# Kernel optimization log

Measured on AMD Instinct MI355X. Metric: run time of the kernel, lower is better.

The kernel has to match this reference:

```python
import jax, jax.numpy as jnp
import numpy as np

B, N, M, C = 1024, 2048, 128, 512
EPS = 1e-8


def setup_inputs() -> dict:
    key = jax.random.key(0)
    k1, k2, k3, k4, k5 = jax.random.split(key, 5)
    x = jax.random.normal(k1, (B, C), dtype=jnp.float32)
    u = jax.random.uniform(k2, (B, N), dtype=jnp.float32) + 1e-3
    w_prev = u / jnp.sum(u, axis=1, keepdims=True)  # valid attention distribution
    mem = jax.random.normal(k3, (B, N, M), dtype=jnp.float32)
    # xavier-uniform-ish fc_read weight (gain 1.4), tiny-std bias
    limit = 1.4 * np.sqrt(6.0 / (C + (M + 6)))
    W = jax.random.uniform(k4, (M + 6, C), dtype=jnp.float32, minval=-limit, maxval=limit)
    b = 0.01 * jax.random.normal(k5, (M + 6,), dtype=jnp.float32)
    return {"x": x, "w_prev": w_prev, "mem": mem, "W": W, "b": b}


def reference(x, w_prev, mem, W, b):
    m = mem.shape[-1]
    o = x @ W.T + b                                   # [B, M+6]
    k = o[:, :m]                                      # key [B, M]
    beta = jax.nn.softplus(o[:, m:m + 1])             # [B, 1]
    g = jax.nn.sigmoid(o[:, m + 1:m + 2])             # [B, 1]
    s = jax.nn.softmax(o[:, m + 2:m + 5], axis=1)     # [B, 3] shift weights
    gamma = 1.0 + jax.nn.softplus(o[:, m + 5:m + 6])  # [B, 1]

    # content addressing: cosine similarity, beta-sharpened softmax
    dot = jnp.einsum('bnm,bm->bn', mem, k)
    denom = jnp.linalg.norm(mem, axis=-1) * jnp.linalg.norm(k, axis=-1, keepdims=True) + EPS
    w_c = jax.nn.softmax(beta * (dot / denom), axis=1)  # [B, N]

    # gate interpolation
    w_g = g * w_c + (1.0 - g) * w_prev

    # circular convolution with 3-tap shift: w_t[i] = sum_j s[j] * w_g[(i+j-1) mod N]
    w_t = (s[:, 0:1] * jnp.roll(w_g, 1, axis=1)
           + s[:, 1:2] * w_g
           + s[:, 2:3] * jnp.roll(w_g, -1, axis=1))

    # sharpening
    w_pow = w_t ** gamma
    w = w_pow / (jnp.sum(w_pow, axis=1, keepdims=True) + 1e-16)

    # weighted read
    r = jnp.einsum('bn,bnm->bm', w, mem)
    return (r, w)
```

## Files before the change

kernel.cpp:

```cpp
#include <hip/hip_runtime.h>
#include <math.h>

#define B 1024
#define N 2048
#define M 128
#define C 512
#define OD (M + 6)
#define EPSF 1e-8f
#define CHUNK 512
#define NCHUNK 4
#define NGRP 64
#define ITERS (B / NGRP)
#define GRID_F (NCHUNK * NGRP)
#define AGENT __HIP_MEMORY_SCOPE_AGENT

__device__ __forceinline__ float softplusf(float x) {
    return fmaxf(x, 0.f) + log1pf(expf(-fabsf(x)));
}
__device__ __forceinline__ float sigmoidf_(float x) {
    return 1.f / (1.f + expf(-x));
}

__device__ __forceinline__ void bar_lds() {
    asm volatile("s_waitcnt lgkmcnt(0)" ::: "memory");
    __builtin_amdgcn_s_barrier();
}

__global__ __launch_bounds__(256) void k_head(
    const float* __restrict__ x, const float* __restrict__ W,
    const float* __restrict__ bias, float* __restrict__ kbuf,
    float* __restrict__ params)
{
    const int b = blockIdx.x;
    __shared__ float xs[C];
    __shared__ float os[OD];
    __shared__ float red[128];

    for (int i = threadIdx.x; i < C; i += 256) xs[i] = x[(size_t)b * C + i];
    __syncthreads();

    if (threadIdx.x < OD) {
        const int j = threadIdx.x;
        const float4* wr = (const float4*)(W + (size_t)j * C);
        float acc = 0.f;
#pragma unroll 8
        for (int c = 0; c < C / 4; ++c) {
            float4 wv = wr[c];
            acc = fmaf(wv.x, xs[4 * c + 0], acc);
            acc = fmaf(wv.y, xs[4 * c + 1], acc);
            acc = fmaf(wv.z, xs[4 * c + 2], acc);
            acc = fmaf(wv.w, xs[4 * c + 3], acc);
        }
        os[j] = acc + bias[j];
    }
    __syncthreads();

    if (threadIdx.x < M) {
        float v = os[threadIdx.x];
        kbuf[(size_t)b * M + threadIdx.x] = v;
        red[threadIdx.x] = v * v;
    }
    __syncthreads();
    for (int s = 64; s > 0; s >>= 1) {
        if (threadIdx.x < s) red[threadIdx.x] += red[threadIdx.x + s];
        __syncthreads();
    }
    if (threadIdx.x == 0) {
        float kn = sqrtf(red[0]);
        float beta = softplusf(os[M]);
        float g = sigmoidf_(os[M + 1]);
        float a0 = os[M + 2], a1 = os[M + 3], a2 = os[M + 4];
        float mx = fmaxf(a0, fmaxf(a1, a2));
        float e0 = expf(a0 - mx), e1 = expf(a1 - mx), e2 = expf(a2 - mx);
        float inv = 1.f / (e0 + e1 + e2);
        float gamma = 1.f + softplusf(os[M + 5]);
        float* p = params + (size_t)b * 8;
        p[0] = beta; p[1] = g; p[2] = e0 * inv; p[3] = e1 * inv;
        p[4] = e2 * inv; p[5] = gamma; p[6] = kn; p[7] = 0.f;
    }
}

__global__ __launch_bounds__(1024, 4) void k_fused(
    const float* __restrict__ mem, const float* __restrict__ kbuf,
    const float* __restrict__ params, const float* __restrict__ w_prev,
    float* __restrict__ w_out,
    float* __restrict__ sPart, float* __restrict__ tPart,
    int* __restrict__ cnt1, float* __restrict__ edgeE,
    float* __restrict__ rpart)
{
    __shared__ float eA[CHUNK];
    __shared__ float wgA[CHUNK + 2];
    __shared__ float pwA[CHUNK];
    __shared__ float redA[16 * 128];
    __shared__ float partS[32];
    __shared__ float partT[8];
    __shared__ float bcast[4];

    const int tid  = threadIdx.x;
    const int lane = tid & 63;
    const int wv   = tid >> 6;
    const int half = lane >> 5;
    const int l32  = lane & 31;
    const int hw   = wv * 2 + half;

    const int cid  = blockIdx.x >> 6;
    const int bgrp = blockIdx.x & 63;

    for (int it = 0; it < ITERS; ++it) {
        const int b = bgrp * ITERS + it;
        const float* cb = mem + ((size_t)b * N + cid * CHUNK) * M;

        float4 frag[16];
#pragma unroll
        for (int j = 0; j < 16; ++j)
            frag[j] = ((const float4*)(cb + (size_t)(hw * 16 + j) * M))[l32];

        float wp_t = 0.f, wpL = 0.f, wpR = 0.f;
        if (tid < CHUNK)
            wp_t = w_prev[(size_t)b * N + cid * CHUNK + tid];
        if (tid == 0) {
            wpL = w_prev[(size_t)b * N + ((cid * CHUNK + N - 1) & (N - 1))];
            wpR = w_prev[(size_t)b * N + ((cid * CHUNK + CHUNK) & (N - 1))];
        }
        const float4 kv = ((const float4*)(kbuf + (size_t)b * M))[l32];
        const float4 p0 = ((const float4*)(params + (size_t)b * 8))[0];
        const float4 p1 = ((const float4*)(params + (size_t)b * 8))[1];
        const float beta = p0.x, kn = p1.z;

        float myS = 0.f;
#pragma unroll
        for (int j = 0; j < 16; ++j) {
            float dot = frag[j].x * kv.x + frag[j].y * kv.y + frag[j].z * kv.z + frag[j].w * kv.w;
            float sq  = frag[j].x * frag[j].x + frag[j].y * frag[j].y + frag[j].z * frag[j].z + frag[j].w * frag[j].w;
#pragma unroll
            for (int s = 16; s >= 1; s >>= 1) {
                dot += __shfl_xor(dot, s, 64);
                sq  += __shfl_xor(sq,  s, 64);
            }
            if (l32 == 0) {
                const float z = beta * dot / (sqrtf(sq) * kn + EPSF);
                const float e = expf(z);
                eA[hw * 16 + j] = e;
                myS += e;
            }
        }
        if (l32 == 0) partS[hw] = myS;
        bar_lds();

        if (tid == 0) {
            float S = 0.f;
#pragma unroll
            for (int h = 0; h < 32; ++h) S += partS[h];
            __hip_atomic_store(&sPart[(size_t)b * NCHUNK + cid], S, __ATOMIC_RELAXED, AGENT);
            __hip_atomic_store(&edgeE[((size_t)b * NCHUNK + cid) * 2 + 0], eA[0], __ATOMIC_RELAXED, AGENT);
            __hip_atomic_store(&edgeE[((size_t)b * NCHUNK + cid) * 2 + 1], eA[CHUNK - 1], __ATOMIC_RELAXED, AGENT);
            asm volatile("s_waitcnt vmcnt(0)" ::: "memory");
            __hip_atomic_fetch_add(&cnt1[b], 1, __ATOMIC_RELAXED, AGENT);
            int tries = 0;
            while (__hip_atomic_load(&cnt1[b], __ATOMIC_RELAXED, AGENT) < NCHUNK) {
                __builtin_amdgcn_s_sleep(1);
                if (++tries > (1 << 22)) break;
            }
            float St = 0.f;
#pragma unroll
            for (int c2 = 0; c2 < NCHUNK; ++c2)
                St += __hip_atomic_load(&sPart[(size_t)b * NCHUNK + c2], __ATOMIC_RELAXED, AGENT);
            bcast[0] = 1.f / St;
            bcast[1] = __hip_atomic_load(&edgeE[((size_t)b * NCHUNK + ((cid + NCHUNK - 1) & (NCHUNK - 1))) * 2 + 1], __ATOMIC_RELAXED, AGENT);
            bcast[2] = __hip_atomic_load(&edgeE[((size_t)b * NCHUNK + ((cid + 1) & (NCHUNK - 1))) * 2 + 0], __ATOMIC_RELAXED, AGENT);
        }
        bar_lds();

        const float invS = bcast[0], eL = bcast[1], eR = bcast[2];
        const float g = p0.y, s0p = p0.z, s1p = p0.w, s2p = p1.x, gamma = p1.y;
        if (tid < CHUNK)
            wgA[tid + 1] = g * eA[tid] * invS + (1.f - g) * wp_t;
        if (tid == 0) {
            wgA[0]         = g * eL * invS + (1.f - g) * wpL;
            wgA[CHUNK + 1] = g * eR * invS + (1.f - g) * wpR;
        }
        bar_lds();

        float myT = 0.f;
        if (tid < CHUNK) {
            const float wt = s0p * wgA[tid] + s1p * wgA[tid + 1] + s2p * wgA[tid + 2];
            const float pw = powf(wt, gamma);
            pwA[tid] = pw;
            myT = pw;
        }
#pragma unroll
        for (int s = 32; s >= 1; s >>= 1) myT += __shfl_xor(myT, s, 64);
        if (lane == 0 && wv < 8) partT[wv] = myT;
        bar_lds();

        if (tid == 0) {
            float T = 0.f;
#pragma unroll
            for (int w2 = 0; w2 < 8; ++w2) T += partT[w2];
            tPart[(size_t)b * NCHUNK + cid] = T;
        }

        float4 acc = make_float4(0.f, 0.f, 0.f, 0.f);
#pragma unroll
        for (int j = 0; j < 16; ++j) {
            const float pw = pwA[hw * 16 + j];
            acc.x = fmaf(pw, frag[j].x, acc.x);
            acc.y = fmaf(pw, frag[j].y, acc.y);
            acc.z = fmaf(pw, frag[j].z, acc.z);
            acc.w = fmaf(pw, frag[j].w, acc.w);
        }
        acc.x += __shfl_xor(acc.x, 32, 64);
        acc.y += __shfl_xor(acc.y, 32, 64);
        acc.z += __shfl_xor(acc.z, 32, 64);
        acc.w += __shfl_xor(acc.w, 32, 64);
        if (half == 0) *(float4*)&redA[wv * 128 + l32 * 4] = acc;
        bar_lds();

        if (tid < 128) {
            float s = 0.f;
#pragma unroll
            for (int w2 = 0; w2 < 16; ++w2) s += redA[w2 * 128 + tid];
            rpart[((size_t)b * NCHUNK + cid) * 128 + tid] = s;
        }
        if (tid < CHUNK)
            w_out[(size_t)b * N + cid * CHUNK + tid] = pwA[tid];
        bar_lds();
    }
}

__global__ __launch_bounds__(256) void k_norm(
    const float* __restrict__ tPart, const float* __restrict__ rpart,
    float* __restrict__ w_out, float* __restrict__ r_out)
{
    const int b = blockIdx.x, tid = threadIdx.x;
    float T = 0.f;
#pragma unroll
    for (int c = 0; c < NCHUNK; ++c) T += tPart[(size_t)b * NCHUNK + c];
    const float invT = 1.f / (T + 1e-16f);

    float4* w4 = (float4*)(w_out + (size_t)b * N);
#pragma unroll
    for (int k = 0; k < 2; ++k) {
        float4 v = w4[tid + k * 256];
        v.x *= invT; v.y *= invT; v.z *= invT; v.w *= invT;
        w4[tid + k * 256] = v;
    }
    if (tid < 128) {
        float s = 0.f;
#pragma unroll
        for (int c = 0; c < NCHUNK; ++c)
            s += rpart[((size_t)b * NCHUNK + c) * 128 + tid];
        r_out[(size_t)b * M + tid] = s * invT;
    }
}

extern "C" void kernel_launch(void* const* d_in, const int* in_sizes, int n_in,
                              void* d_out, int out_size, void* d_ws, size_t ws_size,
                              hipStream_t stream) {
    const float* x      = (const float*)d_in[0];
    const float* w_prev = (const float*)d_in[1];
    const float* mem    = (const float*)d_in[2];
    const float* W      = (const float*)d_in[3];
    const float* bias   = (const float*)d_in[4];

    float* r_out = (float*)d_out;
    float* w_out = (float*)d_out + (size_t)B * M;

    float* ws     = (float*)d_ws;
    float* kbuf   = ws;
    float* params = kbuf + (size_t)B * M;
    float* sPart  = params + (size_t)B * 8;
    float* tPart  = sPart + (size_t)B * NCHUNK;
    int*   cnt1   = (int*)(tPart + (size_t)B * NCHUNK);
    float* edgeE  = (float*)(cnt1 + B);
    float* rpart  = edgeE + (size_t)B * NCHUNK * 2;

    hipMemsetAsync(cnt1, 0, B * sizeof(int), stream);

    k_head<<<B, 256, 0, stream>>>(x, W, bias, kbuf, params);
    k_fused<<<GRID_F, 1024, 0, stream>>>(mem, kbuf, params, w_prev, w_out,
                                         sPart, tPart, cnt1, edgeE, rpart);
    k_norm<<<B, 256, 0, stream>>>(tPart, rpart, w_out, r_out);
}
```

Before: 344.8 us.

## Double-buffer memory fragments across batch rows and halve block size

Each block now prefetches the next batch row's memory fragment, key and params into a second register set while the current row finishes, issuing the loads around the cross-block spin-wait so global latency overlaps the softmax-sum synchronisation. Chunking changes to 8 chunks of 256 rows with 512-thread blocks, keeping 256 blocks that each handle 32 rows. This doubles fragment register pressure (two float4[16] sets) and doubles the number of blocks that must meet at each per-row counter barrier.

```diff
diff --git a/kernel.cpp b/kernel.cpp
--- a/kernel.cpp
+++ b/kernel.cpp
@@ -7,11 +7,11 @@
 #define C 512
 #define OD (M + 6)
 #define EPSF 1e-8f
-#define CHUNK 512
-#define NCHUNK 4
-#define NGRP 64
-#define ITERS (B / NGRP)
-#define GRID_F (NCHUNK * NGRP)
+#define CHUNK 256
+#define NCHUNK 8
+#define NGRP 32
+#define ITERS 32
+#define GRID_F 256
 #define AGENT __HIP_MEMORY_SCOPE_AGENT
 
 __device__ __forceinline__ float softplusf(float x) {
@@ -80,7 +80,134 @@
     }
 }
 
-__global__ __launch_bounds__(1024, 4) void k_fused(
+#define STEP(IT, FC, KC, P0C, P1C, FN, KN_, P0N, P1N)                          \
+{                                                                              \
+    const int b  = bgrp * ITERS + (IT);                                        \
+    const int bn = (b + 1 < B) ? (b + 1) : b;   \
+    float wp_t = 0.f, wpL = 0.f, wpR = 0.f;                                    \
+    if (tid < CHUNK) wp_t = w_prev[(size_t)b * N + cid * CHUNK + tid];         \
+    if (tid == 0) {                                                            \
+        wpL = w_prev[(size_t)b * N + ((cid * CHUNK + N - 1) & (N - 1))];       \
+        wpR = w_prev[(size_t)b * N + ((cid * CHUNK + CHUNK) & (N - 1))];       \
+    }                                                                          \
+    const float beta = P0C.x, kn = P1C.z;                                      \
+                  \
+    float myS = 0.f;                                                           \
+    _Pragma("unroll")                                                          \
+    for (int j = 0; j < 16; ++j) {                                             \
+        float dot = FC[j].x * KC.x + FC[j].y * KC.y + FC[j].z * KC.z + FC[j].w * KC.w; \
+        float sq  = FC[j].x * FC[j].x + FC[j].y * FC[j].y + FC[j].z * FC[j].z + FC[j].w * FC[j].w; \
+        _Pragma("unroll")                                                      \
+        for (int s = 16; s >= 1; s >>= 1) {                                    \
+            dot += __shfl_xor(dot, s, 64);                                     \
+            sq  += __shfl_xor(sq,  s, 64);                                     \
+        }                                                                      \
+        if (l32 == 0) {                                                        \
+            const float z = beta * dot / (sqrtf(sq) * kn + EPSF);              \
+            const float e = expf(z);                                           \
+            eA[hw * 16 + j] = e;                                               \
+            myS += e;                                                          \
+        }                                                                      \
+    }                                                                          \
+    if (l32 == 0) partS[hw] = myS;                                             \
+    bar_lds();                                     \
+      \
+    if (tid == 0) {                                                            \
+        float S = 0.f;                                                         \
+        _Pragma("unroll")                                                      \
+        for (int h = 0; h < 16; ++h) S += partS[h];                            \
+        __hip_atomic_store(&sPart[(size_t)b * NCHUNK + cid], S, __ATOMIC_RELAXED, AGENT); \
+        __hip_atomic_store(&edgeE[((size_t)b * NCHUNK + cid) * 2 + 0], eA[0], __ATOMIC_RELAXED, AGENT); \
+        __hip_atomic_store(&edgeE[((size_t)b * NCHUNK + cid) * 2 + 1], eA[CHUNK - 1], __ATOMIC_RELAXED, AGENT); \
+        asm volatile("s_waitcnt vmcnt(0)" ::: "memory");                       \
+        __hip_atomic_fetch_add(&cnt1[b], 1, __ATOMIC_RELAXED, AGENT);          \
+    }                                                                          \
+     \
+    const float* nb = mem + ((size_t)bn * N + cid * CHUNK) * M;                \
+    if (wv != 0) {                                                             \
+        _Pragma("unroll")                                                      \
+        for (int j = 0; j < 16; ++j)                                           \
+            FN[j] = ((const float4*)(nb + (size_t)(hw * 16 + j) * M))[l32];    \
+        KN_ = ((const float4*)(kbuf + (size_t)bn * M))[l32];                   \
+    }                                                                          \
+    P0N = ((const float4*)(params + (size_t)bn * 8))[0];                       \
+    P1N = ((const float4*)(params + (size_t)bn * 8))[1];                       \
+         \
+    if (tid == 0) {                                                            \
+        int tries = 0;                                                         \
+        while (__hip_atomic_load(&cnt1[b], __ATOMIC_RELAXED, AGENT) < NCHUNK) {\
+            __builtin_amdgcn_s_sleep(1);                                       \
+            if (++tries > (1 << 22)) break;           \
+        }                                                                      \
+        float St = 0.f;                                                        \
+        _Pragma("unroll")                                                      \
+        for (int c2 = 0; c2 < NCHUNK; ++c2)    \
+            St += __hip_atomic_load(&sPart[(size_t)b * NCHUNK + c2], __ATOMIC_RELAXED, AGENT); \
+        bcast[0] = 1.f / St;                                                   \
+        bcast[1] = __hip_atomic_load(&edgeE[((size_t)b * NCHUNK + ((cid + NCHUNK - 1) & (NCHUNK - 1))) * 2 + 1], __ATOMIC_RELAXED, AGENT); \
+        bcast[2] = __hip_atomic_load(&edgeE[((size_t)b * NCHUNK + ((cid + 1) & (NCHUNK - 1))) * 2 + 0], __ATOMIC_RELAXED, AGENT); \
+    }                                                                          \
+    bar_lds();                                        \
+                               \
+    if (wv == 0) {                                                             \
+        _Pragma("unroll")                                                      \
+        for (int j = 0; j < 16; ++j)                                           \
+            FN[j] = ((const float4*)(nb + (size_t)(hw * 16 + j) * M))[l32];    \
+        KN_ = ((const float4*)(kbuf + (size_t)bn * M))[l32];                   \
+    }                                                                          \
+                             \
+    const float invS = bcast[0], eL = bcast[1], eR = bcast[2];                 \
+    const float g = P0C.y, s0p = P0C.z, s1p = P0C.w, s2p = P1C.x, gamma = P1C.y; \
+    if (tid < CHUNK)                                                           \
+        wgA[tid + 1] = g * eA[tid] * invS + (1.f - g) * wp_t;                  \
+    if (tid == 0) {                                                            \
+        wgA[0]         = g * eL * invS + (1.f - g) * wpL;                      \
+        wgA[CHUNK + 1] = g * eR * invS + (1.f - g) * wpR;                      \
+    }                                                                          \
+    bar_lds();                                          \
+    float myT = 0.f;                                                           \
+    if (tid < CHUNK) {                                                         \
+        const float wt = s0p * wgA[tid] + s1p * wgA[tid + 1] + s2p * wgA[tid + 2]; \
+        const float pw = powf(wt, gamma);                                      \
+        pwA[tid] = pw;                                                         \
+        myT = pw;                                                              \
+    }                                                                          \
+    _Pragma("unroll")                                                          \
+    for (int s = 32; s >= 1; s >>= 1) myT += __shfl_xor(myT, s, 64);           \
+    if (lane == 0 && wv < 4) partT[wv] = myT;                                  \
+    bar_lds();                                    \
+    if (tid == 0) {                                                            \
+        tPart[(size_t)b * NCHUNK + cid] = partT[0] + partT[1] + partT[2] + partT[3]; \
+    }                                                                          \
+       \
+    float4 acc = make_float4(0.f, 0.f, 0.f, 0.f);                              \
+    _Pragma("unroll")                                                          \
+    for (int j = 0; j < 16; ++j) {                                             \
+        const float pw = pwA[hw * 16 + j];                                     \
+        acc.x = fmaf(pw, FC[j].x, acc.x);                                      \
+        acc.y = fmaf(pw, FC[j].y, acc.y);                                      \
+        acc.z = fmaf(pw, FC[j].z, acc.z);                                      \
+        acc.w = fmaf(pw, FC[j].w, acc.w);                                      \
+    }                                                                          \
+    acc.x += __shfl_xor(acc.x, 32, 64);                                        \
+    acc.y += __shfl_xor(acc.y, 32, 64);                                        \
+    acc.z += __shfl_xor(acc.z, 32, 64);                                        \
+    acc.w += __shfl_xor(acc.w, 32, 64);                                        \
+    if (half == 0) *(float4*)&redA[wv * 128 + l32 * 4] = acc;                  \
+    bar_lds();                                         \
+    if (tid < 128) {                                                           \
+        float s = 0.f;                                                         \
+        _Pragma("unroll")                                                      \
+        for (int w2 = 0; w2 < 8; ++w2) s += redA[w2 * 128 + tid];              \
+        rpart[((size_t)b * NCHUNK + cid) * 128 + tid] = s;                     \
+    }                                                                          \
+                  \
+    if (tid < CHUNK)                                                           \
+        w_out[(size_t)b * N + cid * CHUNK + tid] = pwA[tid];                   \
+         \
+}
+
+__global__ __launch_bounds__(512, 2) void k_fused(
     const float* __restrict__ mem, const float* __restrict__ kbuf,
     const float* __restrict__ params, const float* __restrict__ w_prev,
     float* __restrict__ w_out,
@@ -91,9 +218,9 @@
     __shared__ float eA[CHUNK];
     __shared__ float wgA[CHUNK + 2];
     __shared__ float pwA[CHUNK];
-    __shared__ float redA[16 * 128];
-    __shared__ float partS[32];
-    __shared__ float partT[8];
+    __shared__ float redA[8 * 128];
+    __shared__ float partS[16];
+    __shared__ float partT[4];
     __shared__ float bcast[4];
 
     const int tid  = threadIdx.x;
@@ -103,128 +230,25 @@
     const int l32  = lane & 31;
     const int hw   = wv * 2 + half;
 
-    const int cid  = blockIdx.x >> 6;
-    const int bgrp = blockIdx.x & 63;
-
-    for (int it = 0; it < ITERS; ++it) {
-        const int b = bgrp * ITERS + it;
-        const float* cb = mem + ((size_t)b * N + cid * CHUNK) * M;
-
-        float4 frag[16];
+    const int cid  = blockIdx.x >> 5;
+    const int bgrp = blockIdx.x & 31;
+
+    float4 fA[16], fB[16], kvA, kvB, p0A, p1A, p0B, p1B;
+
+    {
+        const int b0 = bgrp * ITERS;
+        const float* cb = mem + ((size_t)b0 * N + cid * CHUNK) * M;
 #pragma unroll
         for (int j = 0; j < 16; ++j)
-            frag[j] = ((const float4*)(cb + (size_t)(hw * 16 + j) * M))[l32];
-
-        float wp_t = 0.f, wpL = 0.f, wpR = 0.f;
-        if (tid < CHUNK)
-            wp_t = w_prev[(size_t)b * N + cid * CHUNK + tid];
-        if (tid == 0) {
-            wpL = w_prev[(size_t)b * N + ((cid * CHUNK + N - 1) & (N - 1))];
-            wpR = w_prev[(size_t)b * N + ((cid * CHUNK + CHUNK) & (N - 1))];
-        }
-        const float4 kv = ((const float4*)(kbuf + (size_t)b * M))[l32];
-        const float4 p0 = ((const float4*)(params + (size_t)b * 8))[0];
-        const float4 p1 = ((const float4*)(params + (size_t)b * 8))[1];
-        const float beta = p0.x, kn = p1.z;
-
-        float myS = 0.f;
-#pragma unroll
-        for (int j = 0; j < 16; ++j) {
-            float dot = frag[j].x * kv.x + frag[j].y * kv.y + frag[j].z * kv.z + frag[j].w * kv.w;
-            float sq  = frag[j].x * frag[j].x + frag[j].y * frag[j].y + frag[j].z * frag[j].z + frag[j].w * frag[j].w;
-#pragma unroll
-            for (int s = 16; s >= 1; s >>= 1) {
-                dot += __shfl_xor(dot, s, 64);
-                sq  += __shfl_xor(sq,  s, 64);
-            }
-            if (l32 == 0) {
-                const float z = beta * dot / (sqrtf(sq) * kn + EPSF);
-                const float e = expf(z);
-                eA[hw * 16 + j] = e;
-                myS += e;
-            }
-        }
-        if (l32 == 0) partS[hw] = myS;
-        bar_lds();
-
-        if (tid == 0) {
-            float S = 0.f;
-#pragma unroll
-            for (int h = 0; h < 32; ++h) S += partS[h];
-            __hip_atomic_store(&sPart[(size_t)b * NCHUNK + cid], S, __ATOMIC_RELAXED, AGENT);
-            __hip_atomic_store(&edgeE[((size_t)b * NCHUNK + cid) * 2 + 0], eA[0], __ATOMIC_RELAXED, AGENT);
-            __hip_atomic_store(&edgeE[((size_t)b * NCHUNK + cid) * 2 + 1], eA[CHUNK - 1], __ATOMIC_RELAXED, AGENT);
-            asm volatile("s_waitcnt vmcnt(0)" ::: "memory");
-            __hip_atomic_fetch_add(&cnt1[b], 1, __ATOMIC_RELAXED, AGENT);
-            int tries = 0;
-            while (__hip_atomic_load(&cnt1[b], __ATOMIC_RELAXED, AGENT) < NCHUNK) {
-                __builtin_amdgcn_s_sleep(1);
-                if (++tries > (1 << 22)) break;
-            }
-            float St = 0.f;
-#pragma unroll
-            for (int c2 = 0; c2 < NCHUNK; ++c2)
-                St += __hip_atomic_load(&sPart[(size_t)b * NCHUNK + c2], __ATOMIC_RELAXED, AGENT);
-            bcast[0] = 1.f / St;
-            bcast[1] = __hip_atomic_load(&edgeE[((size_t)b * NCHUNK + ((cid + NCHUNK - 1) & (NCHUNK - 1))) * 2 + 1], __ATOMIC_RELAXED, AGENT);
-            bcast[2] = __hip_atomic_load(&edgeE[((size_t)b * NCHUNK + ((cid + 1) & (NCHUNK - 1))) * 2 + 0], __ATOMIC_RELAXED, AGENT);
-        }
-        bar_lds();
-
-        const float invS = bcast[0], eL = bcast[1], eR = bcast[2];
-        const float g = p0.y, s0p = p0.z, s1p = p0.w, s2p = p1.x, gamma = p1.y;
-        if (tid < CHUNK)
-            wgA[tid + 1] = g * eA[tid] * invS + (1.f - g) * wp_t;
-        if (tid == 0) {
-            wgA[0]         = g * eL * invS + (1.f - g) * wpL;
-            wgA[CHUNK + 1] = g * eR * invS + (1.f - g) * wpR;
-        }
-        bar_lds();
-
-        float myT = 0.f;
-        if (tid < CHUNK) {
-            const float wt = s0p * wgA[tid] + s1p * wgA[tid + 1] + s2p * wgA[tid + 2];
-            const float pw = powf(wt, gamma);
-            pwA[tid] = pw;
-            myT = pw;
-        }
-#pragma unroll
-        for (int s = 32; s >= 1; s >>= 1) myT += __shfl_xor(myT, s, 64);
-        if (lane == 0 && wv < 8) partT[wv] = myT;
-        bar_lds();
-
-        if (tid == 0) {
-            float T = 0.f;
-#pragma unroll
-            for (int w2 = 0; w2 < 8; ++w2) T += partT[w2];
-            tPart[(size_t)b * NCHUNK + cid] = T;
-        }
-
-        float4 acc = make_float4(0.f, 0.f, 0.f, 0.f);
-#pragma unroll
-        for (int j = 0; j < 16; ++j) {
-            const float pw = pwA[hw * 16 + j];
-            acc.x = fmaf(pw, frag[j].x, acc.x);
-            acc.y = fmaf(pw, frag[j].y, acc.y);
-            acc.z = fmaf(pw, frag[j].z, acc.z);
-            acc.w = fmaf(pw, frag[j].w, acc.w);
-        }
-        acc.x += __shfl_xor(acc.x, 32, 64);
-        acc.y += __shfl_xor(acc.y, 32, 64);
-        acc.z += __shfl_xor(acc.z, 32, 64);
-        acc.w += __shfl_xor(acc.w, 32, 64);
-        if (half == 0) *(float4*)&redA[wv * 128 + l32 * 4] = acc;
-        bar_lds();
-
-        if (tid < 128) {
-            float s = 0.f;
-#pragma unroll
-            for (int w2 = 0; w2 < 16; ++w2) s += redA[w2 * 128 + tid];
-            rpart[((size_t)b * NCHUNK + cid) * 128 + tid] = s;
-        }
-        if (tid < CHUNK)
-            w_out[(size_t)b * N + cid * CHUNK + tid] = pwA[tid];
-        bar_lds();
+            fA[j] = ((const float4*)(cb + (size_t)(hw * 16 + j) * M))[l32];
+        kvA = ((const float4*)(kbuf + (size_t)b0 * M))[l32];
+        p0A = ((const float4*)(params + (size_t)b0 * 8))[0];
+        p1A = ((const float4*)(params + (size_t)b0 * 8))[1];
+    }
+
+    for (int it = 0; it < ITERS; it += 2) {
+        STEP(it,     fA, kvA, p0A, p1A, fB, kvB, p0B, p1B)
+        STEP(it + 1, fB, kvB, p0B, p1B, fA, kvA, p0A, p1A)
     }
 }
 
@@ -278,7 +302,7 @@
     hipMemsetAsync(cnt1, 0, B * sizeof(int), stream);
 
     k_head<<<B, 256, 0, stream>>>(x, W, bias, kbuf, params);
-    k_fused<<<GRID_F, 1024, 0, stream>>>(mem, kbuf, params, w_prev, w_out,
-                                         sPart, tPart, cnt1, edgeE, rpart);
+    k_fused<<<GRID_F, 512, 0, stream>>>(mem, kbuf, params, w_prev, w_out,
+                                        sPart, tPart, cnt1, edgeE, rpart);
     k_norm<<<B, 256, 0, stream>>>(tPart, rpart, w_out, r_out);
 }
```

New measurement: 415.7 us. 20.6% more time.
